# Kernel tuning notes

Measured on AMD Instinct MI355X. Metric: run time of the kernel, lower is better.

## Reference

```python
import jax, jax.numpy as jnp
import numpy as np

B, K, N = 8, 4, 131072
DENSITY = 0.3
NEG_PAD = -1000.0
NEG_IDLE = -1.0e8


def setup_inputs() -> dict:
    rng = np.random.default_rng(0)
    mask_s = rng.random((B, K, N)) < DENSITY  # bool, per-slot variable counts
    mask_a = rng.random((B, K, N)) < DENSITY
    ts = int(mask_s.sum())
    ta = int(mask_a.sum())
    key = jax.random.key(0)
    k1, k2, k3, k4 = jax.random.split(key, 4)
    return {
        "rgb": jax.random.normal(k1, (ts, 3), dtype=jnp.float32),
        "logits_surface": jax.random.normal(k2, (ts, 1), dtype=jnp.float32),
        "logits_air": jax.random.normal(k3, (ta, 1), dtype=jnp.float32),
        "idle_states": (jax.random.uniform(k4, (B, K)) < 0.25).astype(jnp.float32),
        "mask_eval_surface": jnp.asarray(mask_s),
        "mask_eval_air": jnp.asarray(mask_a),
    }


def _expand(mask, values):
    # mask: (B,K,N) bool; values: (total, C) packed in row-major (b,k,n) mask order.
    # Returns (B,K,N,C) where masked positions hold their packed value (others garbage,
    # to be overwritten by the caller's jnp.where). Equivalent to the torch B*K scatter loop.
    m = mask.reshape(-1)
    pos = jnp.cumsum(m.astype(jnp.int32)) - 1  # packed index for each masked slot
    pos = jnp.clip(pos, 0, values.shape[0] - 1)
    return jnp.take(values, pos, axis=0).reshape(mask.shape + (values.shape[-1],))


def reference(rgb, logits_surface, logits_air, idle_states,
              mask_eval_surface, mask_eval_air):
    alive = (1.0 - idle_states)[:, :, None, None]  # (B,K,1,1)
    idle = idle_states[:, :, None, None]
    ms = mask_eval_surface[..., None]  # (B,K,N,1)
    ma = mask_eval_air[..., None]

    rgb_out = jnp.where(ms, _expand(mask_eval_surface, rgb) * alive, 0.0)
    logits_surface_out = jnp.where(
        ms, _expand(mask_eval_surface, logits_surface) * alive + idle * NEG_IDLE, NEG_PAD)
    logits_air_out = jnp.where(
        ma, _expand(mask_eval_air, logits_air) * alive + idle * NEG_IDLE, NEG_PAD)
    return rgb_out, logits_surface_out, logits_air_out
```

## Files before the change

### kernel.cpp

```cpp
#include <hip/hip_runtime.h>
#include <stdint.h>

#define NPER      131072
#define NTOT      4194304LL
#define CHUNK     2048
#define NBLK      2048
#define NEG_PAD   (-1000.0f)
#define NEG_IDLE  (-100000000.0f)

typedef unsigned long long u64;

__global__ __launch_bounds__(256, 8) void count_kernel(
    const int* __restrict__ ms, const int* __restrict__ ma,
    unsigned short* __restrict__ cmp, u64* __restrict__ totals)
{
    const int t = threadIdx.x, lane = t & 63, wave = t >> 6;
    const unsigned bid = blockIdx.x;
    const long long base = (long long)bid * CHUNK;

    const int4* ms4 = (const int4*)(ms + base);
    const int4* ma4 = (const int4*)(ma + base);
    int4 s0 = ms4[2 * t], s1 = ms4[2 * t + 1];
    int4 a0 = ma4[2 * t], a1 = ma4[2 * t + 1];
    unsigned sbits = (unsigned)(s0.x != 0)        | ((unsigned)(s0.y != 0) << 1)
                   | ((unsigned)(s0.z != 0) << 2) | ((unsigned)(s0.w != 0) << 3)
                   | ((unsigned)(s1.x != 0) << 4) | ((unsigned)(s1.y != 0) << 5)
                   | ((unsigned)(s1.z != 0) << 6) | ((unsigned)(s1.w != 0) << 7);
    unsigned abits = (unsigned)(a0.x != 0)        | ((unsigned)(a0.y != 0) << 1)
                   | ((unsigned)(a0.z != 0) << 2) | ((unsigned)(a0.w != 0) << 3)
                   | ((unsigned)(a1.x != 0) << 4) | ((unsigned)(a1.y != 0) << 5)
                   | ((unsigned)(a1.z != 0) << 6) | ((unsigned)(a1.w != 0) << 7);

    cmp[bid * 256u + (unsigned)t] = (unsigned short)(sbits | (abits << 8));

    unsigned cnt = __popc(sbits) | (__popc(abits) << 16);
    #pragma unroll
    for (int o = 32; o; o >>= 1) cnt += __shfl_down(cnt, o, 64);
    __shared__ unsigned lds[4];
    if (lane == 0) lds[wave] = cnt;
    __syncthreads();
    if (t == 0) {
        unsigned tot = lds[0] + lds[1] + lds[2] + lds[3];
        totals[bid] = (u64)(tot & 0xffffu) | ((u64)(tot >> 16) << 32);
    }
}

__global__ __launch_bounds__(256, 8) void expand_kernel(
    const float* __restrict__ rgb, const float* __restrict__ lsurf,
    const float* __restrict__ lair, const float* __restrict__ idle,
    const unsigned short* __restrict__ cmp, const u64* __restrict__ totals,
    unsigned rgb_max, unsigned ts_max, unsigned ta_max,
    float* __restrict__ out_rgb, float* __restrict__ out_ls, float* __restrict__ out_la)
{
    __shared__ unsigned wsum[4];
    __shared__ u64 wacc[4];
    __shared__ unsigned packLDS[256];
    __shared__ unsigned prefLDS[256];
    __shared__ float    rgbLDS[3072];

    const int t = threadIdx.x, lane = t & 63, wave = t >> 6;
    const unsigned bid = blockIdx.x;
    const long long base = (long long)bid * CHUNK;

    unsigned pk = cmp[bid * 256u + (unsigned)t];
    u64 acc = 0;
    #pragma unroll
    for (int j = 0; j < 8; ++j) {
        unsigned idx = (unsigned)t * 8u + (unsigned)j;
        acc += (idx < bid) ? totals[idx] : 0ULL;
    }
    const float idle_v = idle[(int)(base >> 17)];

    packLDS[t] = pk;
    unsigned cnt = __popc(pk & 0xffu) | (__popc(pk >> 8) << 16);

    unsigned x = cnt;
    #pragma unroll
    for (int o = 1; o < 64; o <<= 1) {
        unsigned y = __shfl_up(x, o, 64);
        if (lane >= o) x += y;
    }
    if (lane == 63) wsum[wave] = x;
    #pragma unroll
    for (int o = 32; o; o >>= 1) acc += __shfl_down(acc, o, 64);
    if (lane == 0) wacc[wave] = acc;
    __syncthreads();
    unsigned pre = (wave > 0 ? wsum[0] : 0u) + (wave > 1 ? wsum[1] : 0u)
                 + (wave > 2 ? wsum[2] : 0u);
    prefLDS[t] = pre + x - cnt;
    u64 basesum = wacc[0] + wacc[1] + wacc[2] + wacc[3];
    const unsigned excS = (unsigned)(basesum & 0xffffffffULL);
    const unsigned excA = (unsigned)(basesum >> 32);
    __syncthreads();

    const float alive     = 1.0f - idle_v;
    const float idle_term = idle_v * NEG_IDLE;
    const int  sub = t >> 3, b = t & 7;
    const unsigned sm = (1u << b) - 1u;

    #pragma unroll
    for (int h = 0; h < 2; ++h) {
        #pragma unroll
        for (int r = 0; r < 4; ++r) {
            const int e = (h * 4 + r) * 256 + t;
            const int p = ((h * 4 + r) << 5) + sub;
            unsigned w  = packLDS[p];
            unsigned pv = prefLDS[p];
            unsigned rs = excS + (pv & 0xffffu) + __popc(w & sm);
            unsigned ra = excA + (pv >> 16)     + __popc((w >> 8) & sm);
            unsigned s = (w >> b) & 1u, a = (w >> (8 + b)) & 1u;

            float lso = NEG_PAD, lao = NEG_PAD;
            const int li = r * 768 + 3 * t;
            if (s) {
                unsigned pr = rs < rgb_max ? rs : rgb_max;
                long long q = 3LL * pr;
                rgbLDS[li]     = rgb[q]     * alive;
                rgbLDS[li + 1] = rgb[q + 1] * alive;
                rgbLDS[li + 2] = rgb[q + 2] * alive;
                unsigned pl = rs < ts_max ? rs : ts_max;
                lso = lsurf[pl] * alive + idle_term;
            } else {
                rgbLDS[li] = 0.f; rgbLDS[li + 1] = 0.f; rgbLDS[li + 2] = 0.f;
            }
            if (a) {
                unsigned pa = ra < ta_max ? ra : ta_max;
                lao = lair[pa] * alive + idle_term;
            }
            out_ls[base + e] = lso;
            out_la[base + e] = lao;
        }
        __syncthreads();
        float4* dst = (float4*)(out_rgb + 3 * base) + (h ? 768 : 0);
        const float4* src = (const float4*)rgbLDS;
        dst[t]       = src[t];
        dst[t + 256] = src[t + 256];
        dst[t + 512] = src[t + 512];
        __syncthreads();
    }
}

extern "C" void kernel_launch(void* const* d_in, const int* in_sizes, int n_in,
                              void* d_out, int out_size, void* d_ws, size_t ws_size,
                              hipStream_t stream)
{
    const float* rgb   = (const float*)d_in[0];
    const float* lsurf = (const float*)d_in[1];
    const float* lair  = (const float*)d_in[2];
    const float* idle  = (const float*)d_in[3];
    const int*   ms    = (const int*)d_in[4];
    const int*   ma    = (const int*)d_in[5];

    unsigned rgb_max = (unsigned)(in_sizes[0] / 3 - 1);
    unsigned ts_max  = (unsigned)(in_sizes[1] - 1);
    unsigned ta_max  = (unsigned)(in_sizes[2] - 1);

    float* out     = (float*)d_out;
    float* out_rgb = out;
    float* out_ls  = out + NTOT * 3;
    float* out_la  = out_ls + NTOT;

    u64* totals = (u64*)d_ws;
    unsigned short* cmp = (unsigned short*)((char*)d_ws + 16384);

    count_kernel<<<NBLK, 256, 0, stream>>>(ms, ma, cmp, totals);
    expand_kernel<<<NBLK, 256, 0, stream>>>(rgb, lsurf, lair, idle, cmp, totals,
                                            rgb_max, ts_max, ta_max,
                                            out_rgb, out_ls, out_la);
}
```

Measured before the change: 148.9 us.

## Vectorize logit gather and store as float4 per thread, use float3 rgb loads

Logit outputs are now computed four consecutive elements per thread. One unaligned float4 window is loaded from each packed logits array, and the output is written with a single 16-byte store, replacing scalar gathers and scalar stores. RGB gathers use a single 3-float vector load. Occupancy hint is lowered to 6 waves per SIMD to allow more registers. Clamping the window base to ts_max-3 assumes at least four packed values and adds select logic per element.

```diff
diff --git a/kernel.cpp b/kernel.cpp
--- a/kernel.cpp
+++ b/kernel.cpp
@@ -1,7 +1,6 @@
 #include <hip/hip_runtime.h>
 #include <stdint.h>
 
-#define NPER      131072
 #define NTOT      4194304LL
 #define CHUNK     2048
 #define NBLK      2048
@@ -9,6 +8,9 @@
 #define NEG_IDLE  (-100000000.0f)
 
 typedef unsigned long long u64;
+typedef float float4u __attribute__((ext_vector_type(4), aligned(4)));
+typedef float float3u __attribute__((ext_vector_type(3), aligned(4)));
+typedef float float4a __attribute__((ext_vector_type(4), aligned(16)));
 
 __global__ __launch_bounds__(256, 8) void count_kernel(
     const int* __restrict__ ms, const int* __restrict__ ma,
@@ -45,7 +47,7 @@
     }
 }
 
-__global__ __launch_bounds__(256, 8) void expand_kernel(
+__global__ __launch_bounds__(256, 6) void expand_kernel(
     const float* __restrict__ rgb, const float* __restrict__ lsurf,
     const float* __restrict__ lair, const float* __restrict__ idle,
     const unsigned short* __restrict__ cmp, const u64* __restrict__ totals,
@@ -96,43 +98,66 @@
     const float alive     = 1.0f - idle_v;
     const float idle_term = idle_v * NEG_IDLE;
     const int  sub = t >> 3, b = t & 7;
-    const unsigned sm = (1u << b) - 1u;
+    const unsigned bm = (1u << b) - 1u;
+    const int  hp = t >> 1;
+    const unsigned nib = (unsigned)(t & 1) * 4u;
+    const unsigned nm  = (1u << nib) - 1u;
 
     #pragma unroll
     for (int h = 0; h < 2; ++h) {
         #pragma unroll
         for (int r = 0; r < 4; ++r) {
-            const int e = (h * 4 + r) * 256 + t;
-            const int p = ((h * 4 + r) << 5) + sub;
+            const int g = h * 4 + r;
+            const int p = (g << 5) + sub;
             unsigned w  = packLDS[p];
             unsigned pv = prefLDS[p];
-            unsigned rs = excS + (pv & 0xffffu) + __popc(w & sm);
-            unsigned ra = excA + (pv >> 16)     + __popc((w >> 8) & sm);
-            unsigned s = (w >> b) & 1u, a = (w >> (8 + b)) & 1u;
-
-            float lso = NEG_PAD, lao = NEG_PAD;
+            unsigned rs = excS + (pv & 0xffffu) + __popc(w & bm);
             const int li = r * 768 + 3 * t;
-            if (s) {
+            if ((w >> b) & 1u) {
                 unsigned pr = rs < rgb_max ? rs : rgb_max;
-                long long q = 3LL * pr;
-                rgbLDS[li]     = rgb[q]     * alive;
-                rgbLDS[li + 1] = rgb[q + 1] * alive;
-                rgbLDS[li + 2] = rgb[q + 2] * alive;
-                unsigned pl = rs < ts_max ? rs : ts_max;
-                lso = lsurf[pl] * alive + idle_term;
+                float3u v = *(const float3u*)(rgb + 3LL * pr);
+                rgbLDS[li]     = v.x * alive;
+                rgbLDS[li + 1] = v.y * alive;
+                rgbLDS[li + 2] = v.z * alive;
             } else {
                 rgbLDS[li] = 0.f; rgbLDS[li + 1] = 0.f; rgbLDS[li + 2] = 0.f;
             }
-            if (a) {
-                unsigned pa = ra < ta_max ? ra : ta_max;
-                lao = lair[pa] * alive + idle_term;
+        }
+        {
+            const int p = h * 128 + hp;
+            unsigned w  = packLDS[p];
+            unsigned pv = prefLDS[p];
+            unsigned ws = w & 0xffu, wa = (w >> 8) & 0xffu;
+            unsigned r0s = excS + (pv & 0xffffu) + __popc(ws & nm);
+            unsigned r0a = excA + (pv >> 16)     + __popc(wa & nm);
+            unsigned sb = (ws >> nib) & 0xFu;
+            unsigned ab = (wa >> nib) & 0xFu;
+            unsigned rbs = r0s < ts_max - 3u ? r0s : ts_max - 3u;
+            unsigned rba = r0a < ta_max - 3u ? r0a : ta_max - 3u;
+            float4u Ws = *(const float4u*)(lsurf + rbs);
+            float4u Wa = *(const float4u*)(lair  + rba);
+            float lsv[4], lav[4];
+            #pragma unroll
+            for (int j = 0; j < 4; ++j) {
+                unsigned mj = (1u << j) - 1u;
+                unsigned rj = r0s + __popc(sb & mj);
+                unsigned cs = (rj < ts_max ? rj : ts_max) - rbs;
+                float vs = cs == 0 ? Ws.x : cs == 1 ? Ws.y : cs == 2 ? Ws.z : Ws.w;
+                lsv[j] = ((sb >> j) & 1u) ? vs * alive + idle_term : NEG_PAD;
+                unsigned rk = r0a + __popc(ab & mj);
+                unsigned ca = (rk < ta_max ? rk : ta_max) - rba;
+                float va = ca == 0 ? Wa.x : ca == 1 ? Wa.y : ca == 2 ? Wa.z : Wa.w;
+                lav[j] = ((ab >> j) & 1u) ? va * alive + idle_term : NEG_PAD;
             }
-            out_ls[base + e] = lso;
-            out_la[base + e] = lao;
+            const long long eb = base + h * 1024 + 4 * t;
+            float4a vls; vls.x = lsv[0]; vls.y = lsv[1]; vls.z = lsv[2]; vls.w = lsv[3];
+            float4a vla; vla.x = lav[0]; vla.y = lav[1]; vla.z = lav[2]; vla.w = lav[3];
+            *(float4a*)(out_ls + eb) = vls;
+            *(float4a*)(out_la + eb) = vla;
         }
         __syncthreads();
-        float4* dst = (float4*)(out_rgb + 3 * base) + (h ? 768 : 0);
-        const float4* src = (const float4*)rgbLDS;
+        float4a* dst = (float4a*)(out_rgb + 3 * base) + h * 768;
+        const float4a* src = (const float4a*)rgbLDS;
         dst[t]       = src[t];
         dst[t + 256] = src[t + 256];
         dst[t + 512] = src[t + 512];
```

New measurement: 148.0 us, median of 2. Within noise of the previous version (-0.6%).
